# Performance work log

Measured on AMD Instinct MI355X. Metric: run time of the kernel, lower is better.

## Reference

```python
import jax, jax.numpy as jnp
import numpy as np

EPS = 1e-5
NUM_GROUPS = 32
MIN_POINTS = 4

def group_norm(x, gamma, beta):
    # x: [N, C]; torch GroupNorm applied on (1, C, N): normalize each group over (C/G, N)
    N, C = x.shape
    xg = x.reshape(N, NUM_GROUPS, C // NUM_GROUPS)
    mean = jnp.mean(xg, axis=(0, 2), keepdims=True)
    var = jnp.mean((xg - mean) ** 2, axis=(0, 2), keepdims=True)
    xn = (xg - mean) * jax.lax.rsqrt(var + EPS)
    return xn.reshape(N, C) * gamma + beta

def setup_inputs() -> dict:
    key = jax.random.key(0)
    ks = jax.random.split(key, 12)
    N, V = 1000000, 100000
    C0, C = 3, 64  # input feats (minus barycentric col), hidden width
    distributed = jax.random.normal(ks[0], (N, C0 + 1), dtype=jnp.float32)
    indices = jax.random.randint(ks[1], (N,), 0, V, dtype=jnp.int32)
    # kaiming_normal fan_in, relu: std = sqrt(2 / fan_in)
    W0 = jax.random.normal(ks[2], (C, C0), dtype=jnp.float32) * np.sqrt(2.0 / C0)
    W1 = jax.random.normal(ks[3], (C, C), dtype=jnp.float32) * np.sqrt(2.0 / C)
    W2 = jax.random.normal(ks[4], (C, C), dtype=jnp.float32) * np.sqrt(2.0 / C)
    b2 = jnp.zeros((C,), dtype=jnp.float32)
    g0 = jnp.ones((C,), dtype=jnp.float32)
    beta0 = jnp.zeros((C,), dtype=jnp.float32)
    g1 = jnp.ones((C,), dtype=jnp.float32)
    beta1 = jnp.zeros((C,), dtype=jnp.float32)
    return {"distributed": distributed, "indices": indices, "num_vertices": V,
            "W0": W0, "W1": W1, "W2": W2, "b2": b2,
            "g0": g0, "beta0": beta0, "g1": g1, "beta1": beta1}

def reference(distributed, indices, num_vertices, W0, W1, W2, b2, g0, beta0, g1, beta1):
    N = distributed.shape[0]
    V = int(num_vertices)
    bary = distributed[:, -1]            # [N]
    x = distributed[:, :-1]              # [N, C0]
    # layer 0: linear (no bias) -> GN -> relu
    x = jax.nn.relu(group_norm(x @ W0.T, g0, beta0))
    # layer 1: linear (no bias) -> GN -> relu
    x = jax.nn.relu(group_norm(x @ W1.T, g1, beta1))
    # layer 2 (last): linear with bias -> relu (no norm)
    x = jax.nn.relu(x @ W2.T + b2)       # [N, C]
    idx = jnp.maximum(indices.astype(jnp.int32), 0)
    # scatter-max pooling into lattice vertices
    seg_max = jax.ops.segment_max(x, idx, num_segments=V)          # [V, C], -inf for empty
    seg_max = jnp.where(jnp.isneginf(seg_max), 0.0, seg_max)
    counts = jax.ops.segment_sum(jnp.ones((N,), x.dtype), idx, num_segments=V)  # [V]
    # argmax recovery: first point index attaining the per-segment max, per channel
    gathered_max = seg_max[idx]                                    # [N, C]
    cand = jnp.where(x == gathered_max, jnp.arange(N, dtype=jnp.int32)[:, None], N)
    argmax = jax.ops.segment_min(cand, idx, num_segments=V)        # [V, C]
    argmax = jnp.minimum(argmax, N - 1)
    bary_reduced = bary[argmax]                                    # [V, C]
    out = jnp.concatenate([seg_max, bary_reduced], axis=1)         # [V, 2C]
    few = (counts < MIN_POINTS)[:, None]
    return jnp.where(few, 0.0, out)
```

## Files before the change

### kernel.cpp

```cpp
#include <hip/hip_runtime.h>
#include <hip/hip_bf16.h>
#include <math.h>

#define MIN_POINTS 4

#define WS_W0P   0
#define WS_B0P   768
#define WS_W1P   1024
#define WS_B1P   17408
#define WS_CNT   17920
#define WS_P0    417920
#define WS_P1    548992
#define NPART    1024

__device__ __forceinline__ void waitlgkm(){ asm volatile("s_waitcnt lgkmcnt(0)" ::: "memory"); }

__global__ void k_stats0(const float4* __restrict__ d4, const int* __restrict__ idx,
                         double* __restrict__ partial0, int* __restrict__ cnt, int N){
  __shared__ double red[4][16];
  int tid = blockIdx.x*blockDim.x + threadIdx.x;
  int stride = gridDim.x*blockDim.x;
  double a[9] = {0,0,0,0,0,0,0,0,0};
  for (int i = tid; i < N; i += stride){
    float4 d = d4[i];
    double x0 = d.x, x1 = d.y, x2 = d.z;
    a[0] += x0; a[1] += x1; a[2] += x2;
    a[3] = fma(x0,x0,a[3]); a[4] = fma(x0,x1,a[4]); a[5] = fma(x0,x2,a[5]);
    a[6] = fma(x1,x1,a[6]); a[7] = fma(x1,x2,a[7]); a[8] = fma(x2,x2,a[8]);
    int v = idx[i]; if (v < 0) v = 0;
    atomicAdd(&cnt[v], 1);
  }
  int lane = threadIdx.x & 63, wid = threadIdx.x >> 6;
  #pragma unroll
  for (int j = 0; j < 9; j++){
    double v = a[j];
    for (int o = 32; o > 0; o >>= 1) v += __shfl_down(v, o, 64);
    if (lane == 0) red[wid][j] = v;
  }
  __syncthreads();
  if (threadIdx.x < 9){
    double s = red[0][threadIdx.x] + red[1][threadIdx.x]
             + red[2][threadIdx.x] + red[3][threadIdx.x];
    partial0[blockIdx.x*16 + threadIdx.x] = s;
  }
}

__global__ void k_fold0(const double* __restrict__ partial0, const float* __restrict__ W0,
                        const float* __restrict__ g0, const float* __restrict__ bt0,
                        float* __restrict__ w0p, float* __restrict__ b0p, int N, int nparts){
  __shared__ double sred[16];
  int t = threadIdx.x, lane = t & 63, g = t >> 6;
  if (g < 9){
    double s = 0.0;
    for (int b = lane; b < nparts; b += 64) s += partial0[b*16 + g];
    for (int o = 32; o > 0; o >>= 1) s += __shfl_down(s, o, 64);
    if (lane == 0) sred[g] = s;
  }
  __syncthreads();
  if (t < 64){
    int c = t;
    double sx0 = sred[0], sx1 = sred[1], sx2 = sred[2];
    double G00 = sred[3], G01 = sred[4], G02 = sred[5], G11 = sred[6], G12 = sred[7], G22 = sred[8];
    double s[2], q[2];
    int chans[2] = { c, c ^ 1 };
    #pragma unroll
    for (int u = 0; u < 2; u++){
      int ch = chans[u];
      double w0 = W0[ch*3+0], w1 = W0[ch*3+1], w2 = W0[ch*3+2];
      s[u] = w0*sx0 + w1*sx1 + w2*sx2;
      q[u] = w0*w0*G00 + w1*w1*G11 + w2*w2*G22 + 2.0*(w0*w1*G01 + w0*w2*G02 + w1*w2*G12);
    }
    double inv  = 1.0 / (2.0 * (double)N);
    double mean = (s[0] + s[1]) * inv;
    double var  = (q[0] + q[1]) * inv - mean*mean;
    double aa   = (1.0 / sqrt(var + 1e-5)) * (double)g0[c];
    b0p[c] = (float)((double)bt0[c] - mean * aa);
    w0p[c*3+0] = (float)((double)W0[c*3+0] * aa);
    w0p[c*3+1] = (float)((double)W0[c*3+1] * aa);
    w0p[c*3+2] = (float)((double)W0[c*3+2] * aa);
  }
}

__global__ __launch_bounds__(128, 2)
void k_stats1(const float4* __restrict__ d4,
              const float* __restrict__ w0p, const float* __restrict__ b0p,
              const float* __restrict__ W1, double* __restrict__ part1,
              int N, int ntiles){
  __shared__ float lds[2][16][64][4];
  __shared__ double lds2[2][128];
  int lane = threadIdx.x & 63;
  int wid  = threadIdx.x >> 6;
  float w1r[64];
  #pragma unroll
  for (int k = 0; k < 64; k += 4){
    float4 t = *(const float4*)&W1[lane*64 + k];
    w1r[k] = t.x; w1r[k+1] = t.y; w1r[k+2] = t.z; w1r[k+3] = t.w;
  }
  double s0 = 0.0, s1 = 0.0;
  int gw = blockIdx.x*2 + wid, nw = gridDim.x*2;
  for (int t = gw; t < ntiles; t += nw){
    int rb = t * 64;
    int row = rb + lane;
    float4 d = (row < N) ? d4[row] : make_float4(0.f,0.f,0.f,0.f);
    waitlgkm();
    #pragma unroll
    for (int cg = 0; cg < 16; cg++){
      float hv[4];
      #pragma unroll
      for (int u = 0; u < 4; u++){
        int c = cg*4 + u;
        float t0 = fmaf(w0p[c*3+2], d.z, fmaf(w0p[c*3+1], d.y, fmaf(w0p[c*3+0], d.x, b0p[c])));
        hv[u] = fmaxf(t0, 0.f);
      }
      float4 h4; h4.x = hv[0]; h4.y = hv[1]; h4.z = hv[2]; h4.w = hv[3];
      *(float4*)&lds[wid][cg][lane][0] = h4;
    }
    waitlgkm();
    int rmax = min(64, N - rb);
    for (int r = 0; r < rmax; r++){
      float a0 = 0.f, a1 = 0.f, a2 = 0.f, a3 = 0.f;
      #pragma unroll
      for (int kb = 0; kb < 16; kb++){
        float4 h = *(const float4*)&lds[wid][kb][r][0];
        a0 = fmaf(w1r[kb*4+0], h.x, a0);
        a1 = fmaf(w1r[kb*4+1], h.y, a1);
        a2 = fmaf(w1r[kb*4+2], h.z, a2);
        a3 = fmaf(w1r[kb*4+3], h.w, a3);
      }
      double y = (double)((a0 + a1) + (a2 + a3));
      s0 += y;
      s1 = fma(y, y, s1);
    }
  }
  lds2[wid][lane]      = s0;
  lds2[wid][64 + lane] = s1;
  __syncthreads();
  if (threadIdx.x < 128)
    part1[blockIdx.x*128 + threadIdx.x] = lds2[0][threadIdx.x] + lds2[1][threadIdx.x];
}

__global__ void k_fold1(const double* __restrict__ part1, const float* __restrict__ W1,
                        const float* __restrict__ g1, const float* __restrict__ bt1,
                        float* __restrict__ w1p, float* __restrict__ b1p, int N, int nparts){
  __shared__ double sst[128];
  int t = threadIdx.x;
  int s = t >> 3, j = t & 7;
  double acc = 0.0;
  for (int b = j; b < nparts; b += 8) acc += part1[b*128 + s];
  acc += __shfl_down(acc, 4, 8);
  acc += __shfl_down(acc, 2, 8);
  acc += __shfl_down(acc, 1, 8);
  if (j == 0) sst[s] = acc;
  __syncthreads();
  if (t < 64){
    int c = t, p = c ^ 1;
    double inv  = 1.0 / (2.0 * (double)N);
    double mean = (sst[c] + sst[p]) * inv;
    double Ey2  = (sst[64+c] + sst[64+p]) * inv;
    double var  = Ey2 - mean*mean;
    double a    = (1.0 / sqrt(var + 1e-5)) * (double)g1[c];
    b1p[c] = (float)((double)bt1[c] - mean * a);
    for (int k = 0; k < 64; k++)
      w1p[c*64 + k] = (float)((double)W1[c*64 + k] * a);
  }
}

__global__ __launch_bounds__(128, 2)
void k_main(const float4* __restrict__ d4, const int* __restrict__ idx,
            const float* __restrict__ w0p, const float* __restrict__ b0p,
            const float* __restrict__ w1p, const float* __restrict__ b1p,
            const float* __restrict__ W2,  const float* __restrict__ b2,
            unsigned long long* __restrict__ seg, int N, int ntiles){
  __shared__ float lds[2][16][64][4];
  __shared__ float scr[2][2][64];
  int lane = threadIdx.x & 63;
  int wid  = threadIdx.x >> 6;
  float w1r[64], w2r[64];
  #pragma unroll
  for (int k = 0; k < 64; k += 4){
    float4 t1 = *(const float4*)&w1p[lane*64 + k];
    w1r[k] = t1.x; w1r[k+1] = t1.y; w1r[k+2] = t1.z; w1r[k+3] = t1.w;
    float4 t2 = *(const float4*)&W2[lane*64 + k];
    w2r[k] = t2.x; w2r[k+1] = t2.y; w2r[k+2] = t2.z; w2r[k+3] = t2.w;
  }
  float b1v = b1p[lane], b2v = b2[lane];
  int gw = blockIdx.x*2 + wid, nw = gridDim.x*2;
  for (int t = gw; t < ntiles; t += nw){
    int rb = t * 64;
    int row = rb + lane;
    float4 d = (row < N) ? d4[row] : make_float4(0.f,0.f,0.f,0.f);
    int myv = 0;
    if (row < N){ int v = idx[row]; myv = (v < 0) ? 0 : v; }
    waitlgkm();
    #pragma unroll
    for (int cg = 0; cg < 16; cg++){
      float hv[4];
      #pragma unroll
      for (int u = 0; u < 4; u++){
        int c = cg*4 + u;
        float t0 = fmaf(w0p[c*3+2], d.z, fmaf(w0p[c*3+1], d.y, fmaf(w0p[c*3+0], d.x, b0p[c])));
        hv[u] = fmaxf(t0, 0.f);
      }
      float4 h4; h4.x = hv[0]; h4.y = hv[1]; h4.z = hv[2]; h4.w = hv[3];
      *(float4*)&lds[wid][cg][lane][0] = h4;
    }
    waitlgkm();
    int rmax = min(64, N - rb);
    for (int r = 0; r < rmax; r++){
      int v = __builtin_amdgcn_readlane(myv, r);
      float a0 = b1v, a1 = 0.f, a2 = 0.f, a3 = 0.f;
      #pragma unroll
      for (int kb = 0; kb < 16; kb++){
        float4 h = *(const float4*)&lds[wid][kb][r][0];
        a0 = fmaf(w1r[kb*4+0], h.x, a0);
        a1 = fmaf(w1r[kb*4+1], h.y, a1);
        a2 = fmaf(w1r[kb*4+2], h.z, a2);
        a3 = fmaf(w1r[kb*4+3], h.w, a3);
      }
      float h1 = fmaxf((a0 + a1) + (a2 + a3), 0.f);
      scr[wid][r & 1][lane] = h1;
      waitlgkm();
      float c0 = b2v, c1 = 0.f, c2 = 0.f, c3 = 0.f;
      #pragma unroll
      for (int kb = 0; kb < 16; kb++){
        float4 h = *(const float4*)&scr[wid][r & 1][kb*4];
        c0 = fmaf(w2r[kb*4+0], h.x, c0);
        c1 = fmaf(w2r[kb*4+1], h.y, c1);
        c2 = fmaf(w2r[kb*4+2], h.z, c2);
        c3 = fmaf(w2r[kb*4+3], h.w, c3);
      }
      float h2 = fmaxf((c0 + c1) + (c2 + c3), 0.f);
      unsigned int bits = __float_as_uint(h2) & 0x7fffffffu;
      unsigned long long packed =
          ((unsigned long long)bits << 32) | (unsigned long long)(unsigned int)(~(unsigned int)(rb + r));
      atomicMax(&seg[(size_t)v*64 + lane], packed);
    }
  }
}

__global__ void k_out(const float4* __restrict__ d4, const int* __restrict__ cnt,
                      float* __restrict__ out, int N, int V){
  int lane = threadIdx.x & 63;
  int w = (int)((blockIdx.x*blockDim.x + threadIdx.x) >> 6);
  if (w >= V) return;
  const unsigned long long* seg = (const unsigned long long*)out;
  unsigned long long p = seg[(size_t)w*64 + lane];
  int c = cnt[w];
  unsigned int bits = (unsigned int)(p >> 32);
  unsigned int rowu = ~(unsigned int)p;
  unsigned int nm1 = (unsigned int)(N - 1);
  if (rowu > nm1) rowu = nm1;
  float val  = __uint_as_float(bits);
  float bary = d4[rowu].w;
  bool few = (c < MIN_POINTS);
  float o0 = few ? 0.f : val;
  float o1 = few ? 0.f : bary;
  out[(size_t)w*128 + lane]      = o0;
  out[(size_t)w*128 + 64 + lane] = o1;
}

extern "C" void kernel_launch(void* const* d_in, const int* in_sizes, int n_in,
                              void* d_out, int out_size, void* d_ws, size_t ws_size,
                              hipStream_t stream) {
  const float4* d4  = (const float4*)d_in[0];
  const int*    idx = (const int*)d_in[1];
  const float*  W0  = (const float*)d_in[3];
  const float*  W1  = (const float*)d_in[4];
  const float*  W2  = (const float*)d_in[5];
  const float*  b2  = (const float*)d_in[6];
  const float*  g0  = (const float*)d_in[7];
  const float*  bt0 = (const float*)d_in[8];
  const float*  g1  = (const float*)d_in[9];
  const float*  bt1 = (const float*)d_in[10];

  int N = in_sizes[0] / 4;
  int V = out_size / 128;
  int ntiles = (N + 63) / 64;

  char* ws = (char*)d_ws;
  float*  w0p = (float*)(ws + WS_W0P);
  float*  b0p = (float*)(ws + WS_B0P);
  float*  w1p = (float*)(ws + WS_W1P);
  float*  b1p = (float*)(ws + WS_B1P);
  int*    cnt = (int*)(ws + WS_CNT);
  double* p0  = (double*)(ws + WS_P0);
  double* p1  = (double*)(ws + WS_P1);

  hipMemsetAsync(cnt, 0, (size_t)V * sizeof(int), stream);
  hipMemsetAsync(d_out, 0, (size_t)out_size * sizeof(float), stream);

  k_stats0<<<NPART, 256, 0, stream>>>(d4, idx, p0, cnt, N);
  k_fold0 <<<1, 1024, 0, stream>>>(p0, W0, g0, bt0, w0p, b0p, N, NPART);
  k_stats1<<<NPART, 128, 0, stream>>>(d4, w0p, b0p, W1, p1, N, ntiles);
  k_fold1 <<<1, 1024, 0, stream>>>(p1, W1, g1, bt1, w1p, b1p, N, NPART);
  k_main  <<<NPART, 128, 0, stream>>>(d4, idx, w0p, b0p, w1p, b1p, W2, b2,
                                      (unsigned long long*)d_out, N, ntiles);
  k_out   <<<(V + 3) / 4, 256, 0, stream>>>(d4, cnt, (float*)d_out, N, V);
}
```

Before: 671.6 us.

## Restructure MLP kernels: per-lane row activations with wave-uniform weight loads

k_stats1 and k_main now keep one point's hidden vector per lane in registers. Each wave computes 16 output channels using wave-uniform (scalar-loadable) weight reads, instead of holding a per-lane weight row and looping over 64 rows serially. Blocks go from 2 to 4 waves cooperating on a 64-row tile, with padded LDS transposes between layers and before the atomics. The goal is to cut the serial per-row LDS broadcast and reduction latency and to free the weight registers. The cost is more block-level barriers and a larger h0/h1 register array per lane. w0p is also switched to a channel-major layout.

```diff
diff --git a/kernel.cpp b/kernel.cpp
--- a/kernel.cpp
+++ b/kernel.cpp
@@ -12,8 +12,6 @@
 #define WS_P0    417920
 #define WS_P1    548992
 #define NPART    1024
-
-__device__ __forceinline__ void waitlgkm(){ asm volatile("s_waitcnt lgkmcnt(0)" ::: "memory"); }
 
 __global__ void k_stats0(const float4* __restrict__ d4, const int* __restrict__ idx,
                          double* __restrict__ partial0, int* __restrict__ cnt, int N){
@@ -75,68 +73,70 @@
     double var  = (q[0] + q[1]) * inv - mean*mean;
     double aa   = (1.0 / sqrt(var + 1e-5)) * (double)g0[c];
     b0p[c] = (float)((double)bt0[c] - mean * aa);
-    w0p[c*3+0] = (float)((double)W0[c*3+0] * aa);
-    w0p[c*3+1] = (float)((double)W0[c*3+1] * aa);
-    w0p[c*3+2] = (float)((double)W0[c*3+2] * aa);
-  }
-}
-
-__global__ __launch_bounds__(128, 2)
+    w0p[c]       = (float)((double)W0[c*3+0] * aa);
+    w0p[64 + c]  = (float)((double)W0[c*3+1] * aa);
+    w0p[128 + c] = (float)((double)W0[c*3+2] * aa);
+  }
+}
+
+__global__ __launch_bounds__(256, 4)
 void k_stats1(const float4* __restrict__ d4,
               const float* __restrict__ w0p, const float* __restrict__ b0p,
               const float* __restrict__ W1, double* __restrict__ part1,
               int N, int ntiles){
-  __shared__ float lds[2][16][64][4];
-  __shared__ double lds2[2][128];
+  __shared__ float buf[64][67];
+  __shared__ double red[4][128];
   int lane = threadIdx.x & 63;
-  int wid  = threadIdx.x >> 6;
-  float w1r[64];
-  #pragma unroll
-  for (int k = 0; k < 64; k += 4){
-    float4 t = *(const float4*)&W1[lane*64 + k];
-    w1r[k] = t.x; w1r[k+1] = t.y; w1r[k+2] = t.z; w1r[k+3] = t.w;
-  }
+  int wid  = __builtin_amdgcn_readfirstlane((int)(threadIdx.x >> 6));
+  int cbase = wid * 16;
   double s0 = 0.0, s1 = 0.0;
-  int gw = blockIdx.x*2 + wid, nw = gridDim.x*2;
-  for (int t = gw; t < ntiles; t += nw){
+  for (int t = blockIdx.x; t < ntiles; t += gridDim.x){
     int rb = t * 64;
     int row = rb + lane;
     float4 d = (row < N) ? d4[row] : make_float4(0.f,0.f,0.f,0.f);
-    waitlgkm();
-    #pragma unroll
-    for (int cg = 0; cg < 16; cg++){
-      float hv[4];
-      #pragma unroll
-      for (int u = 0; u < 4; u++){
-        int c = cg*4 + u;
-        float t0 = fmaf(w0p[c*3+2], d.z, fmaf(w0p[c*3+1], d.y, fmaf(w0p[c*3+0], d.x, b0p[c])));
-        hv[u] = fmaxf(t0, 0.f);
-      }
-      float4 h4; h4.x = hv[0]; h4.y = hv[1]; h4.z = hv[2]; h4.w = hv[3];
-      *(float4*)&lds[wid][cg][lane][0] = h4;
-    }
-    waitlgkm();
-    int rmax = min(64, N - rb);
-    for (int r = 0; r < rmax; r++){
+    float h0[64];
+    #pragma unroll
+    for (int c = 0; c < 64; c++){
+      float t0 = b0p[c];
+      t0 = fmaf(w0p[c],       d.x, t0);
+      t0 = fmaf(w0p[64 + c],  d.y, t0);
+      t0 = fmaf(w0p[128 + c], d.z, t0);
+      h0[c] = fmaxf(t0, 0.f);
+    }
+    __syncthreads();
+    #pragma unroll
+    for (int u = 0; u < 16; u++){
+      int co = cbase + u;
+      const float* wr = &W1[co*64];
       float a0 = 0.f, a1 = 0.f, a2 = 0.f, a3 = 0.f;
       #pragma unroll
-      for (int kb = 0; kb < 16; kb++){
-        float4 h = *(const float4*)&lds[wid][kb][r][0];
-        a0 = fmaf(w1r[kb*4+0], h.x, a0);
-        a1 = fmaf(w1r[kb*4+1], h.y, a1);
-        a2 = fmaf(w1r[kb*4+2], h.z, a2);
-        a3 = fmaf(w1r[kb*4+3], h.w, a3);
-      }
-      double y = (double)((a0 + a1) + (a2 + a3));
-      s0 += y;
-      s1 = fma(y, y, s1);
-    }
-  }
-  lds2[wid][lane]      = s0;
-  lds2[wid][64 + lane] = s1;
-  __syncthreads();
-  if (threadIdx.x < 128)
-    part1[blockIdx.x*128 + threadIdx.x] = lds2[0][threadIdx.x] + lds2[1][threadIdx.x];
+      for (int k = 0; k < 64; k += 4){
+        a0 = fmaf(wr[k+0], h0[k+0], a0);
+        a1 = fmaf(wr[k+1], h0[k+1], a1);
+        a2 = fmaf(wr[k+2], h0[k+2], a2);
+        a3 = fmaf(wr[k+3], h0[k+3], a3);
+      }
+      buf[co][lane] = (a0 + a1) + (a2 + a3);
+    }
+    __syncthreads();
+    int rmax = min(64, N - rb);
+    for (int rr = 0; rr < 16; rr++){
+      int r = cbase + rr;
+      if (r < rmax){
+        double y = (double)buf[lane][r];
+        s0 += y;
+        s1 = fma(y, y, s1);
+      }
+    }
+  }
+  __syncthreads();
+  red[wid][lane]      = s0;
+  red[wid][64 + lane] = s1;
+  __syncthreads();
+  if (threadIdx.x < 128){
+    int t = threadIdx.x;
+    part1[blockIdx.x*128 + t] = red[0][t] + red[1][t] + red[2][t] + red[3][t];
+  }
 }
 
 __global__ void k_fold1(const double* __restrict__ part1, const float* __restrict__ W1,
@@ -165,75 +165,77 @@
   }
 }
 
-__global__ __launch_bounds__(128, 2)
+__global__ __launch_bounds__(256, 4)
 void k_main(const float4* __restrict__ d4, const int* __restrict__ idx,
             const float* __restrict__ w0p, const float* __restrict__ b0p,
             const float* __restrict__ w1p, const float* __restrict__ b1p,
             const float* __restrict__ W2,  const float* __restrict__ b2,
             unsigned long long* __restrict__ seg, int N, int ntiles){
-  __shared__ float lds[2][16][64][4];
-  __shared__ float scr[2][2][64];
+  __shared__ float bufH[64][67];
+  __shared__ float bufY[64][67];
   int lane = threadIdx.x & 63;
-  int wid  = threadIdx.x >> 6;
-  float w1r[64], w2r[64];
-  #pragma unroll
-  for (int k = 0; k < 64; k += 4){
-    float4 t1 = *(const float4*)&w1p[lane*64 + k];
-    w1r[k] = t1.x; w1r[k+1] = t1.y; w1r[k+2] = t1.z; w1r[k+3] = t1.w;
-    float4 t2 = *(const float4*)&W2[lane*64 + k];
-    w2r[k] = t2.x; w2r[k+1] = t2.y; w2r[k+2] = t2.z; w2r[k+3] = t2.w;
-  }
-  float b1v = b1p[lane], b2v = b2[lane];
-  int gw = blockIdx.x*2 + wid, nw = gridDim.x*2;
-  for (int t = gw; t < ntiles; t += nw){
+  int wid  = __builtin_amdgcn_readfirstlane((int)(threadIdx.x >> 6));
+  int cbase = wid * 16;
+  for (int t = blockIdx.x; t < ntiles; t += gridDim.x){
     int rb = t * 64;
     int row = rb + lane;
     float4 d = (row < N) ? d4[row] : make_float4(0.f,0.f,0.f,0.f);
     int myv = 0;
     if (row < N){ int v = idx[row]; myv = (v < 0) ? 0 : v; }
-    waitlgkm();
-    #pragma unroll
-    for (int cg = 0; cg < 16; cg++){
-      float hv[4];
+    float h0[64];
+    #pragma unroll
+    for (int c = 0; c < 64; c++){
+      float t0 = b0p[c];
+      t0 = fmaf(w0p[c],       d.x, t0);
+      t0 = fmaf(w0p[64 + c],  d.y, t0);
+      t0 = fmaf(w0p[128 + c], d.z, t0);
+      h0[c] = fmaxf(t0, 0.f);
+    }
+    __syncthreads();
+    #pragma unroll
+    for (int u = 0; u < 16; u++){
+      int co = cbase + u;
+      const float* wr = &w1p[co*64];
+      float a0 = b1p[co], a1 = 0.f, a2 = 0.f, a3 = 0.f;
       #pragma unroll
-      for (int u = 0; u < 4; u++){
-        int c = cg*4 + u;
-        float t0 = fmaf(w0p[c*3+2], d.z, fmaf(w0p[c*3+1], d.y, fmaf(w0p[c*3+0], d.x, b0p[c])));
-        hv[u] = fmaxf(t0, 0.f);
-      }
-      float4 h4; h4.x = hv[0]; h4.y = hv[1]; h4.z = hv[2]; h4.w = hv[3];
-      *(float4*)&lds[wid][cg][lane][0] = h4;
-    }
-    waitlgkm();
+      for (int k = 0; k < 64; k += 4){
+        a0 = fmaf(wr[k+0], h0[k+0], a0);
+        a1 = fmaf(wr[k+1], h0[k+1], a1);
+        a2 = fmaf(wr[k+2], h0[k+2], a2);
+        a3 = fmaf(wr[k+3], h0[k+3], a3);
+      }
+      bufH[co][lane] = fmaxf((a0 + a1) + (a2 + a3), 0.f);
+    }
+    __syncthreads();
+    float h1[64];
+    #pragma unroll
+    for (int k = 0; k < 64; k++) h1[k] = bufH[k][lane];
+    #pragma unroll
+    for (int u = 0; u < 16; u++){
+      int co = cbase + u;
+      const float* wr = &W2[co*64];
+      float a0 = b2[co], a1 = 0.f, a2 = 0.f, a3 = 0.f;
+      #pragma unroll
+      for (int k = 0; k < 64; k += 4){
+        a0 = fmaf(wr[k+0], h1[k+0], a0);
+        a1 = fmaf(wr[k+1], h1[k+1], a1);
+        a2 = fmaf(wr[k+2], h1[k+2], a2);
+        a3 = fmaf(wr[k+3], h1[k+3], a3);
+      }
+      bufY[co][lane] = fmaxf((a0 + a1) + (a2 + a3), 0.f);
+    }
+    __syncthreads();
     int rmax = min(64, N - rb);
-    for (int r = 0; r < rmax; r++){
-      int v = __builtin_amdgcn_readlane(myv, r);
-      float a0 = b1v, a1 = 0.f, a2 = 0.f, a3 = 0.f;
-      #pragma unroll
-      for (int kb = 0; kb < 16; kb++){
-        float4 h = *(const float4*)&lds[wid][kb][r][0];
-        a0 = fmaf(w1r[kb*4+0], h.x, a0);
-        a1 = fmaf(w1r[kb*4+1], h.y, a1);
-        a2 = fmaf(w1r[kb*4+2], h.z, a2);
-        a3 = fmaf(w1r[kb*4+3], h.w, a3);
-      }
-      float h1 = fmaxf((a0 + a1) + (a2 + a3), 0.f);
-      scr[wid][r & 1][lane] = h1;
-      waitlgkm();
-      float c0 = b2v, c1 = 0.f, c2 = 0.f, c3 = 0.f;
-      #pragma unroll
-      for (int kb = 0; kb < 16; kb++){
-        float4 h = *(const float4*)&scr[wid][r & 1][kb*4];
-        c0 = fmaf(w2r[kb*4+0], h.x, c0);
-        c1 = fmaf(w2r[kb*4+1], h.y, c1);
-        c2 = fmaf(w2r[kb*4+2], h.z, c2);
-        c3 = fmaf(w2r[kb*4+3], h.w, c3);
-      }
-      float h2 = fmaxf((c0 + c1) + (c2 + c3), 0.f);
-      unsigned int bits = __float_as_uint(h2) & 0x7fffffffu;
-      unsigned long long packed =
-          ((unsigned long long)bits << 32) | (unsigned long long)(unsigned int)(~(unsigned int)(rb + r));
-      atomicMax(&seg[(size_t)v*64 + lane], packed);
+    for (int rr = 0; rr < 16; rr++){
+      int r = cbase + rr;
+      if (r < rmax){
+        float y = bufY[lane][r];
+        int v = __builtin_amdgcn_readlane(myv, r);
+        unsigned int bits = __float_as_uint(y) & 0x7fffffffu;
+        unsigned long long packed = ((unsigned long long)bits << 32)
+            | (unsigned long long)(unsigned int)(~(unsigned int)(rb + r));
+        atomicMax(&seg[(size_t)v*64 + lane], packed);
+      }
     }
   }
 }
@@ -291,9 +293,9 @@
 
   k_stats0<<<NPART, 256, 0, stream>>>(d4, idx, p0, cnt, N);
   k_fold0 <<<1, 1024, 0, stream>>>(p0, W0, g0, bt0, w0p, b0p, N, NPART);
-  k_stats1<<<NPART, 128, 0, stream>>>(d4, w0p, b0p, W1, p1, N, ntiles);
+  k_stats1<<<NPART, 256, 0, stream>>>(d4, w0p, b0p, W1, p1, N, ntiles);
   k_fold1 <<<1, 1024, 0, stream>>>(p1, W1, g1, bt1, w1p, b1p, N, NPART);
-  k_main  <<<NPART, 128, 0, stream>>>(d4, idx, w0p, b0p, w1p, b1p, W2, b2,
+  k_main  <<<NPART, 256, 0, stream>>>(d4, idx, w0p, b0p, w1p, b1p, W2, b2,
                                       (unsigned long long*)d_out, N, ntiles);
   k_out   <<<(V + 3) / 4, 256, 0, stream>>>(d4, cnt, (float*)d_out, N, V);
 }
```

Measured after the change: 1.328 ms. 1.98x slower.
